# Kernel tuning notes

Measured on AMD Instinct MI355X. Metric: run time of the kernel, lower is better.

## Reference

```python
import jax, jax.numpy as jnp
import numpy as np

EMBED = 1024
HEADS = 16
HEAD_DIM = EMBED // HEADS


def setup_inputs() -> dict:
    key = jax.random.key(0)
    ks = jax.random.split(key, 8)
    B, S = 2, 2048
    inp = {
        "values": jax.random.normal(ks[0], (B, S, EMBED), jnp.float32),
        "keys": jax.random.normal(ks[1], (B, S, EMBED), jnp.float32),
        "queries": jax.random.normal(ks[2], (B, S, EMBED), jnp.float32),
        # per-head projection weights (torch Linear: y = x @ W.T), shared across heads
        "Wv": jax.random.normal(ks[3], (HEAD_DIM, HEAD_DIM), jnp.float32) / np.sqrt(HEAD_DIM),
        "Wk": jax.random.normal(ks[4], (HEAD_DIM, HEAD_DIM), jnp.float32) / np.sqrt(HEAD_DIM),
        "Wq": jax.random.normal(ks[5], (HEAD_DIM, HEAD_DIM), jnp.float32) / np.sqrt(HEAD_DIM),
        "Wo": jax.random.normal(ks[6], (EMBED, EMBED), jnp.float32) / np.sqrt(EMBED),
        "bo": jax.random.normal(ks[7], (EMBED,), jnp.float32) * 0.02,
    }
    return inp


def reference(values, keys, queries, Wv, Wk, Wq, Wo, bo):
    B, S, _ = queries.shape
    # split heads: (B, H, S, D)
    def split(x):
        return x.reshape(B, -1, HEADS, HEAD_DIM).transpose(0, 2, 1, 3)
    v, k, q = split(values), split(keys), split(queries)
    # per-head linear projections (no bias): x @ W.T
    v = jnp.einsum('bhsd,ed->bhse', v, Wv)
    k = jnp.einsum('bhsd,ed->bhse', k, Wk)
    q = jnp.einsum('bhsd,ed->bhse', q, Wq)
    # scaled dot-product attention (naive, full matrix)
    scores = jnp.einsum('bhqd,bhkd->bhqk', q, k) / jnp.sqrt(jnp.float32(HEAD_DIM))
    attn = jax.nn.softmax(scores, axis=-1)
    out = jnp.einsum('bhqk,bhkd->bhqd', attn, v)
    # merge heads and output projection
    out = out.transpose(0, 2, 1, 3).reshape(B, S, EMBED)
    return out @ Wo.T + bo
```

## Files before the change

### kernel.cpp

```cpp
#include <hip/hip_runtime.h>
#include <stdint.h>

#define HEADS 16
#define HD    64
#define SEQ   2048
#define BATCH 2
#define EMB   1024

using short8  = __attribute__((ext_vector_type(8))) short;
using float4v = __attribute__((ext_vector_type(4))) float;
using f32x16  = __attribute__((ext_vector_type(16))) float;

__device__ __forceinline__ unsigned int f2bfr(float f) {
    return (__float_as_uint(f) + 0x8000u) >> 16;
}

__device__ __forceinline__ unsigned int cvt_pk_bf16(float lo, float hi) {
    unsigned int r;
    asm("v_cvt_pk_bf16_f32 %0, %1, %2" : "=v"(r) : "v"(lo), "v"(hi));
    return r;
}

__device__ __forceinline__ short8 mk8(unsigned int a, unsigned int b,
                                      unsigned int c, unsigned int d) {
    union { unsigned int u[4]; short8 s; } x;
    x.u[0] = a; x.u[1] = b; x.u[2] = c; x.u[3] = d;
    return x.s;
}

__global__ __launch_bounds__(256) void cvt_wo_kernel(const float* __restrict__ Wo,
                                                     unsigned short* __restrict__ Wob) {
    int i = (blockIdx.x * 256 + threadIdx.x) * 4;
    float4 v = *(const float4*)(Wo + i);
    uint2 o;
    o.x = f2bfr(v.x) | (f2bfr(v.y) << 16);
    o.y = f2bfr(v.z) | (f2bfr(v.w) << 16);
    *(uint2*)(Wob + i) = o;
}

__global__ __launch_bounds__(256) void proj_kernel(
    const float* __restrict__ Vx, const float* __restrict__ Kx, const float* __restrict__ Qx,
    const float* __restrict__ Wv, const float* __restrict__ Wk, const float* __restrict__ Wq,
    unsigned short* __restrict__ Qp, unsigned short* __restrict__ Kp,
    unsigned short* __restrict__ Vt) {
    __shared__ __align__(16) unsigned short Ws[64 * 72];
    __shared__ __align__(16) unsigned short xs[64 * 72];
    __shared__ __align__(16) unsigned short vt2[64 * 72];

    const int t = threadIdx.x, w = t >> 6, lane = t & 63, cl = lane & 15, quad = lane >> 4;
    const int z  = blockIdx.z;
    const int bh = blockIdx.y;
    const int b  = bh >> 4, h = bh & 15;
    const int s0 = blockIdx.x * 64;

    const float* x = (z == 0) ? Qx : (z == 1) ? Kx : Vx;
    const float* W = (z == 0) ? Wq : (z == 1) ? Wk : Wv;
    const float scale = (z == 0) ? 0.18033688011112044f : 1.0f;

#pragma unroll
    for (int rep = 0; rep < 4; ++rep) {
        int idx = rep * 1024 + t * 4;
        int e = idx >> 6, d0 = idx & 63;
        float4 w4 = *(const float4*)(W + idx);
        uint2 pk;
        pk.x = f2bfr(w4.x * scale) | (f2bfr(w4.y * scale) << 16);
        pk.y = f2bfr(w4.z * scale) | (f2bfr(w4.w * scale) << 16);
        *(uint2*)(&Ws[e * 72 + d0]) = pk;

        int s = e;
        float4 v4 = *(const float4*)(x + (size_t)(b * SEQ + s0 + s) * EMB + h * 64 + d0);
        uint2 px;
        px.x = f2bfr(v4.x) | (f2bfr(v4.y) << 16);
        px.y = f2bfr(v4.z) | (f2bfr(v4.w) << 16);
        *(uint2*)(&xs[s * 72 + d0]) = px;
    }
    __syncthreads();

    short8 a0 = *(const short8*)(&xs[(w * 16 + cl) * 72 + quad * 8]);
    short8 a1 = *(const short8*)(&xs[(w * 16 + cl) * 72 + 32 + quad * 8]);
    float4v c[4];
#pragma unroll
    for (int nt = 0; nt < 4; ++nt) c[nt] = (float4v){0.f, 0.f, 0.f, 0.f};
#pragma unroll
    for (int nt = 0; nt < 4; ++nt) {
        short8 b0 = *(const short8*)(&Ws[(nt * 16 + cl) * 72 + quad * 8]);
        c[nt] = __builtin_amdgcn_mfma_f32_16x16x32_bf16(a0, b0, c[nt], 0, 0, 0);
        short8 b1 = *(const short8*)(&Ws[(nt * 16 + cl) * 72 + 32 + quad * 8]);
        c[nt] = __builtin_amdgcn_mfma_f32_16x16x32_bf16(a1, b1, c[nt], 0, 0, 0);
    }

    if (z < 2) {
#pragma unroll
        for (int nt = 0; nt < 4; ++nt)
#pragma unroll
            for (int r = 0; r < 4; ++r)
                xs[(w * 16 + quad * 4 + r) * 72 + nt * 16 + cl] =
                    (unsigned short)f2bfr(c[nt][r]);
        unsigned short* outp = (z == 0) ? Qp : Kp;
        int sl = w * 16 + (lane >> 2), c0 = (lane & 3) * 16;
        uint4 o0 = *(const uint4*)(&xs[sl * 72 + c0]);
        uint4 o1 = *(const uint4*)(&xs[sl * 72 + c0 + 8]);
        size_t base = ((size_t)bh * SEQ + s0 + sl) * 64 + c0;
        *(uint4*)(outp + base)     = o0;
        *(uint4*)(outp + base + 8) = o1;
    } else {
#pragma unroll
        for (int nt = 0; nt < 4; ++nt)
#pragma unroll
            for (int r = 0; r < 4; ++r)
                vt2[(nt * 16 + cl) * 72 + w * 16 + quad * 4 + r] =
                    (unsigned short)f2bfr(c[nt][r]);
        __syncthreads();
        int e = t >> 2, sc0 = (t & 3) * 16;
        uint4 o0 = *(const uint4*)(&vt2[e * 72 + sc0]);
        uint4 o1 = *(const uint4*)(&vt2[e * 72 + sc0 + 8]);
        size_t base = ((size_t)bh * 64 + e) * SEQ + s0 + sc0;
        *(uint4*)(Vt + base)     = o0;
        *(uint4*)(Vt + base + 8) = o1;
    }
}

__global__ __launch_bounds__(256) void attn_kernel(
    const unsigned short* __restrict__ Qp, const unsigned short* __restrict__ Kp,
    const unsigned short* __restrict__ Vt, unsigned short* __restrict__ AO) {
    __shared__ __align__(16) unsigned short Ks[2][64 * 72];
    __shared__ __align__(16) unsigned short Vs[2][64 * 72];

    const int t = threadIdx.x;
    const int w = t >> 6, lane = t & 63;
    const int l31 = lane & 31, h = lane >> 5;

    const int lid = blockIdx.x;
    const int bh  = ((lid & 7) << 2) | ((lid >> 3) & 3);
    const int q0  = (lid >> 5) * 128;

    const size_t hbase = (size_t)bh * SEQ * 64;
    const unsigned short* Kbase = Kp + hbase;
    const unsigned short* Vbase = Vt + hbase;

    short8 qf[4];
    {
        const unsigned short* qr = Qp + hbase + (size_t)(q0 + w * 32 + l31) * 64 + h * 8;
#pragma unroll
        for (int dt = 0; dt < 4; ++dt) qf[dt] = *(const short8*)(qr + dt * 16);
    }

    short8 ones;
#pragma unroll
    for (int i = 0; i < 8; ++i) ones[i] = (short)0x3F80;

    f32x16 o0, o1, ls;
#pragma unroll
    for (int r = 0; r < 16; ++r) { o0[r] = 0.f; o1[r] = 0.f; ls[r] = 0.f; }

    const int srow = t >> 3;
    const int scol = (t & 7) * 8;

    uint4 kreg[2], vreg[2];
#pragma unroll
    for (int p = 0; p < 2; ++p) {
        int row = srow + p * 32;
        kreg[p] = *(const uint4*)(Kbase + row * 64 + scol);
        vreg[p] = *(const uint4*)(Vbase + (size_t)row * SEQ + scol);
    }

    for (int kc = 0; kc < SEQ / 64; ++kc) {
        const int buf = kc & 1;
#pragma unroll
        for (int p = 0; p < 2; ++p) {
            int row = srow + p * 32;
            *(uint4*)(&Ks[buf][row * 72 + scol]) = kreg[p];
            *(uint4*)(&Vs[buf][row * 72 + scol]) = vreg[p];
        }
        __syncthreads();
        if (kc + 1 < SEQ / 64) {
#pragma unroll
            for (int p = 0; p < 2; ++p) {
                int row = srow + p * 32;
                kreg[p] = *(const uint4*)(Kbase + (size_t)(kc + 1) * 4096 + row * 64 + scol);
                vreg[p] = *(const uint4*)(Vbase + (size_t)row * SEQ + (kc + 1) * 64 + scol);
            }
        }

        f32x16 s0, s1;
#pragma unroll
        for (int r = 0; r < 16; ++r) { s0[r] = 0.f; s1[r] = 0.f; }

        __builtin_amdgcn_s_setprio(1);
#pragma unroll
        for (int dt = 0; dt < 4; ++dt) {
            short8 k0 = *(const short8*)(&Ks[buf][l31 * 72 + dt * 16 + h * 8]);
            short8 k1 = *(const short8*)(&Ks[buf][(32 + l31) * 72 + dt * 16 + h * 8]);
            s0 = __builtin_amdgcn_mfma_f32_32x32x16_bf16(k0, qf[dt], s0, 0, 0, 0);
            s1 = __builtin_amdgcn_mfma_f32_32x32x16_bf16(k1, qf[dt], s1, 0, 0, 0);
        }
        __builtin_amdgcn_s_setprio(0);

#pragma unroll
        for (int r = 0; r < 16; ++r) {
            s0[r] = __builtin_amdgcn_exp2f(s0[r]);
            s1[r] = __builtin_amdgcn_exp2f(s1[r]);
        }

        short8 fr[4];
        {
            unsigned e0 = cvt_pk_bf16(s0[0],  s0[1]),  e1 = cvt_pk_bf16(s0[2],  s0[3]);
            unsigned e2 = cvt_pk_bf16(s0[4],  s0[5]),  e3 = cvt_pk_bf16(s0[6],  s0[7]);
            unsigned e4 = cvt_pk_bf16(s0[8],  s0[9]),  e5 = cvt_pk_bf16(s0[10], s0[11]);
            unsigned e6 = cvt_pk_bf16(s0[12], s0[13]), e7 = cvt_pk_bf16(s0[14], s0[15]);
            unsigned x0 = __shfl_xor(e0, 32), x1 = __shfl_xor(e1, 32);
            unsigned x2 = __shfl_xor(e2, 32), x3 = __shfl_xor(e3, 32);
            unsigned x4 = __shfl_xor(e4, 32), x5 = __shfl_xor(e5, 32);
            unsigned x6 = __shfl_xor(e6, 32), x7 = __shfl_xor(e7, 32);
            fr[0] = mk8(h ? x2 : e0, h ? x3 : e1, h ? e2 : x0, h ? e3 : x1);
            fr[1] = mk8(h ? x6 : e4, h ? x7 : e5, h ? e6 : x4, h ? e7 : x5);
        }
        {
            unsigned e0 = cvt_pk_bf16(s1[0],  s1[1]),  e1 = cvt_pk_bf16(s1[2],  s1[3]);
            unsigned e2 = cvt_pk_bf16(s1[4],  s1[5]),  e3 = cvt_pk_bf16(s1[6],  s1[7]);
            unsigned e4 = cvt_pk_bf16(s1[8],  s1[9]),  e5 = cvt_pk_bf16(s1[10], s1[11]);
            unsigned e6 = cvt_pk_bf16(s1[12], s1[13]), e7 = cvt_pk_bf16(s1[14], s1[15]);
            unsigned x0 = __shfl_xor(e0, 32), x1 = __shfl_xor(e1, 32);
            unsigned x2 = __shfl_xor(e2, 32), x3 = __shfl_xor(e3, 32);
            unsigned x4 = __shfl_xor(e4, 32), x5 = __shfl_xor(e5, 32);
            unsigned x6 = __shfl_xor(e6, 32), x7 = __shfl_xor(e7, 32);
            fr[2] = mk8(h ? x2 : e0, h ? x3 : e1, h ? e2 : x0, h ? e3 : x1);
            fr[3] = mk8(h ? x6 : e4, h ? x7 : e5, h ? e6 : x4, h ? e7 : x5);
        }

        __builtin_amdgcn_s_setprio(1);
#pragma unroll
        for (int c = 0; c < 4; ++c) {
            short8 bv0 = *(const short8*)(&Vs[buf][l31 * 72 + c * 16 + h * 8]);
            short8 bv1 = *(const short8*)(&Vs[buf][(32 + l31) * 72 + c * 16 + h * 8]);
            o0 = __builtin_amdgcn_mfma_f32_32x32x16_bf16(fr[c], bv0, o0, 0, 0, 0);
            o1 = __builtin_amdgcn_mfma_f32_32x32x16_bf16(fr[c], bv1, o1, 0, 0, 0);
            ls = __builtin_amdgcn_mfma_f32_32x32x16_bf16(fr[c], ones,  ls, 0, 0, 0);
        }
        __builtin_amdgcn_s_setprio(0);
    }

    float inv[16];
#pragma unroll
    for (int r = 0; r < 16; ++r) inv[r] = 1.0f / ls[r];
#pragma unroll
    for (int r = 0; r < 16; ++r) {
        int row = q0 + w * 32 + (r & 3) + 8 * (r >> 2) + 4 * h;
        size_t rb = hbase + (size_t)row * 64 + l31;
        AO[rb]      = (unsigned short)f2bfr(o0[r] * inv[r]);
        AO[rb + 32] = (unsigned short)f2bfr(o1[r] * inv[r]);
    }
}

__global__ __launch_bounds__(256) void outproj_kernel(
    const unsigned short* __restrict__ AO, const unsigned short* __restrict__ Wob,
    const float* __restrict__ bo, float* __restrict__ out) {
    const int t = threadIdx.x, w = t >> 6, lane = t & 63;
    const int l31 = lane & 31, h = lane >> 5;

    const int wid = blockIdx.x * 4 + w;
    const int mt  = wid >> 4;
    const int et  = wid & 15;
    const int m0  = mt * 32, e0 = et * 64;
    const int b   = m0 >> 11;
    const int s   = (m0 & 2047) + l31;

    const unsigned short* pA  = AO + ((size_t)(b * 16) * SEQ + s) * 64 + h * 8;
    const unsigned short* pB0 = Wob + (size_t)(e0 + l31) * EMB + h * 8;
    const unsigned short* pB1 = Wob + (size_t)(e0 + 32 + l31) * EMB + h * 8;

    f32x16 c0, c1;
#pragma unroll
    for (int r = 0; r < 16; ++r) { c0[r] = 0.f; c1[r] = 0.f; }

    for (int hh = 0; hh < 16; ++hh) {
#pragma unroll
        for (int k4 = 0; k4 < 4; ++k4) {
            short8 a  = *(const short8*)(pA + k4 * 16);
            short8 b0 = *(const short8*)(pB0 + hh * 64 + k4 * 16);
            short8 b1 = *(const short8*)(pB1 + hh * 64 + k4 * 16);
            c0 = __builtin_amdgcn_mfma_f32_32x32x16_bf16(a, b0, c0, 0, 0, 0);
            c1 = __builtin_amdgcn_mfma_f32_32x32x16_bf16(a, b1, c1, 0, 0, 0);
        }
        pA += (size_t)SEQ * 64;
    }

    const float bias0 = bo[e0 + l31];
    const float bias1 = bo[e0 + 32 + l31];
#pragma unroll
    for (int r = 0; r < 16; ++r) {
        int m = m0 + (r & 3) + 8 * (r >> 2) + 4 * h;
        out[(size_t)m * EMB + e0 + l31]      = c0[r] + bias0;
        out[(size_t)m * EMB + e0 + 32 + l31] = c1[r] + bias1;
    }
}

extern "C" void kernel_launch(void* const* d_in, const int* in_sizes, int n_in,
                              void* d_out, int out_size, void* d_ws, size_t ws_size,
                              hipStream_t stream) {
    const float* values  = (const float*)d_in[0];
    const float* keys    = (const float*)d_in[1];
    const float* queries = (const float*)d_in[2];
    const float* Wv = (const float*)d_in[3];
    const float* Wk = (const float*)d_in[4];
    const float* Wq = (const float*)d_in[5];
    const float* Wo = (const float*)d_in[6];
    const float* bo = (const float*)d_in[7];
    float* out = (float*)d_out;

    char* ws = (char*)d_ws;
    unsigned short* Qp  = (unsigned short*)(ws);
    unsigned short* Kp  = (unsigned short*)(ws + (8u  << 20));
    unsigned short* Vt  = (unsigned short*)(ws + (16u << 20));
    unsigned short* AO  = (unsigned short*)(ws + (24u << 20));
    unsigned short* Wob = (unsigned short*)(ws + (32u << 20));

    cvt_wo_kernel<<<dim3(1024), dim3(256), 0, stream>>>(Wo, Wob);
    proj_kernel<<<dim3(SEQ / 64, BATCH * HEADS, 3), dim3(256), 0, stream>>>(
        values, keys, queries, Wv, Wk, Wq, Qp, Kp, Vt);
    attn_kernel<<<dim3((SEQ / 128) * BATCH * HEADS), dim3(256), 0, stream>>>(Qp, Kp, Vt, AO);
    outproj_kernel<<<dim3((EMB / 64) * ((BATCH * SEQ) / 32) / 4), dim3(256), 0, stream>>>(
        AO, Wob, bo, out);
}
```

Baseline: 231.3 us.

## Rewrite projection kernel as per-wave 32x32 MFMA tiles without shared memory

The projection kernel now gives each wave its own 32-row sequence tile. Each wave loads the input and weight fragments straight from global memory into registers, converts them to bf16 with the packed convert instruction, and uses 32x32x16 MFMAs. This removes the LDS staging, the __syncthreads barriers and the shared-memory transpose for V. In exchange, the outputs are written as scattered 2-byte stores, and every wave reloads the full 64x64 weight matrix from global memory.

```diff
diff --git a/kernel.cpp b/kernel.cpp
--- a/kernel.cpp
+++ b/kernel.cpp
@@ -43,80 +43,78 @@
     const float* __restrict__ Wv, const float* __restrict__ Wk, const float* __restrict__ Wq,
     unsigned short* __restrict__ Qp, unsigned short* __restrict__ Kp,
     unsigned short* __restrict__ Vt) {
-    __shared__ __align__(16) unsigned short Ws[64 * 72];
-    __shared__ __align__(16) unsigned short xs[64 * 72];
-    __shared__ __align__(16) unsigned short vt2[64 * 72];
-
-    const int t = threadIdx.x, w = t >> 6, lane = t & 63, cl = lane & 15, quad = lane >> 4;
-    const int z  = blockIdx.z;
-    const int bh = blockIdx.y;
-    const int b  = bh >> 4, h = bh & 15;
-    const int s0 = blockIdx.x * 64;
+    const int t = threadIdx.x, w = t >> 6, lane = t & 63;
+    const int l31 = lane & 31, h = lane >> 5;
+
+    const int wid  = blockIdx.x * 4 + w;
+    const int z    = wid >> 11;
+    const int rest = wid & 2047;
+    const int bh   = rest >> 6;
+    const int s0   = (rest & 63) * 32;
+    const int b    = bh >> 4, hh = bh & 15;
 
     const float* x = (z == 0) ? Qx : (z == 1) ? Kx : Vx;
     const float* W = (z == 0) ? Wq : (z == 1) ? Wk : Wv;
     const float scale = (z == 0) ? 0.18033688011112044f : 1.0f;
 
-#pragma unroll
-    for (int rep = 0; rep < 4; ++rep) {
-        int idx = rep * 1024 + t * 4;
-        int e = idx >> 6, d0 = idx & 63;
-        float4 w4 = *(const float4*)(W + idx);
-        uint2 pk;
-        pk.x = f2bfr(w4.x * scale) | (f2bfr(w4.y * scale) << 16);
-        pk.y = f2bfr(w4.z * scale) | (f2bfr(w4.w * scale) << 16);
-        *(uint2*)(&Ws[e * 72 + d0]) = pk;
-
-        int s = e;
-        float4 v4 = *(const float4*)(x + (size_t)(b * SEQ + s0 + s) * EMB + h * 64 + d0);
-        uint2 px;
-        px.x = f2bfr(v4.x) | (f2bfr(v4.y) << 16);
-        px.y = f2bfr(v4.z) | (f2bfr(v4.w) << 16);
-        *(uint2*)(&xs[s * 72 + d0]) = px;
-    }
-    __syncthreads();
-
-    short8 a0 = *(const short8*)(&xs[(w * 16 + cl) * 72 + quad * 8]);
-    short8 a1 = *(const short8*)(&xs[(w * 16 + cl) * 72 + 32 + quad * 8]);
-    float4v c[4];
-#pragma unroll
-    for (int nt = 0; nt < 4; ++nt) c[nt] = (float4v){0.f, 0.f, 0.f, 0.f};
-#pragma unroll
-    for (int nt = 0; nt < 4; ++nt) {
-        short8 b0 = *(const short8*)(&Ws[(nt * 16 + cl) * 72 + quad * 8]);
-        c[nt] = __builtin_amdgcn_mfma_f32_16x16x32_bf16(a0, b0, c[nt], 0, 0, 0);
-        short8 b1 = *(const short8*)(&Ws[(nt * 16 + cl) * 72 + 32 + quad * 8]);
-        c[nt] = __builtin_amdgcn_mfma_f32_16x16x32_bf16(a1, b1, c[nt], 0, 0, 0);
-    }
+    const float* xr = x + ((size_t)(b * SEQ + s0 + l31)) * EMB + hh * 64 + h * 8;
+    short8 xf[4];
+#pragma unroll
+    for (int dt = 0; dt < 4; ++dt) {
+        const float* p = xr + dt * 16;
+        float4 u = *(const float4*)p;
+        float4 v = *(const float4*)(p + 4);
+        xf[dt] = mk8(cvt_pk_bf16(u.x, u.y), cvt_pk_bf16(u.z, u.w),
+                     cvt_pk_bf16(v.x, v.y), cvt_pk_bf16(v.z, v.w));
+    }
+
+    short8 wf[2][4];
+#pragma unroll
+    for (int et = 0; et < 2; ++et) {
+        const float* wr = W + (size_t)(et * 32 + l31) * 64 + h * 8;
+#pragma unroll
+        for (int dt = 0; dt < 4; ++dt) {
+            const float* p = wr + dt * 16;
+            float4 u = *(const float4*)p;
+            float4 v = *(const float4*)(p + 4);
+            wf[et][dt] = mk8(cvt_pk_bf16(u.x * scale, u.y * scale),
+                             cvt_pk_bf16(u.z * scale, u.w * scale),
+                             cvt_pk_bf16(v.x * scale, v.y * scale),
+                             cvt_pk_bf16(v.z * scale, v.w * scale));
+        }
+    }
+
+    f32x16 c0, c1;
+#pragma unroll
+    for (int r = 0; r < 16; ++r) { c0[r] = 0.f; c1[r] = 0.f; }
 
     if (z < 2) {
 #pragma unroll
-        for (int nt = 0; nt < 4; ++nt)
-#pragma unroll
-            for (int r = 0; r < 4; ++r)
-                xs[(w * 16 + quad * 4 + r) * 72 + nt * 16 + cl] =
-                    (unsigned short)f2bfr(c[nt][r]);
+        for (int dt = 0; dt < 4; ++dt) {
+            c0 = __builtin_amdgcn_mfma_f32_32x32x16_bf16(xf[dt], wf[0][dt], c0, 0, 0, 0);
+            c1 = __builtin_amdgcn_mfma_f32_32x32x16_bf16(xf[dt], wf[1][dt], c1, 0, 0, 0);
+        }
         unsigned short* outp = (z == 0) ? Qp : Kp;
-        int sl = w * 16 + (lane >> 2), c0 = (lane & 3) * 16;
-        uint4 o0 = *(const uint4*)(&xs[sl * 72 + c0]);
-        uint4 o1 = *(const uint4*)(&xs[sl * 72 + c0 + 8]);
-        size_t base = ((size_t)bh * SEQ + s0 + sl) * 64 + c0;
-        *(uint4*)(outp + base)     = o0;
-        *(uint4*)(outp + base + 8) = o1;
+        size_t base = ((size_t)bh * SEQ + s0) * 64;
+#pragma unroll
+        for (int r = 0; r < 16; ++r) {
+            int sr = (r & 3) + 8 * (r >> 2) + 4 * h;
+            outp[base + (size_t)sr * 64 + l31]      = (unsigned short)f2bfr(c0[r]);
+            outp[base + (size_t)sr * 64 + 32 + l31] = (unsigned short)f2bfr(c1[r]);
+        }
     } else {
 #pragma unroll
-        for (int nt = 0; nt < 4; ++nt)
-#pragma unroll
-            for (int r = 0; r < 4; ++r)
-                vt2[(nt * 16 + cl) * 72 + w * 16 + quad * 4 + r] =
-                    (unsigned short)f2bfr(c[nt][r]);
-        __syncthreads();
-        int e = t >> 2, sc0 = (t & 3) * 16;
-        uint4 o0 = *(const uint4*)(&vt2[e * 72 + sc0]);
-        uint4 o1 = *(const uint4*)(&vt2[e * 72 + sc0 + 8]);
-        size_t base = ((size_t)bh * 64 + e) * SEQ + s0 + sc0;
-        *(uint4*)(Vt + base)     = o0;
-        *(uint4*)(Vt + base + 8) = o1;
+        for (int dt = 0; dt < 4; ++dt) {
+            c0 = __builtin_amdgcn_mfma_f32_32x32x16_bf16(wf[0][dt], xf[dt], c0, 0, 0, 0);
+            c1 = __builtin_amdgcn_mfma_f32_32x32x16_bf16(wf[1][dt], xf[dt], c1, 0, 0, 0);
+        }
+        size_t base = (size_t)bh * 64 * SEQ + s0;
+#pragma unroll
+        for (int r = 0; r < 16; ++r) {
+            int er = (r & 3) + 8 * (r >> 2) + 4 * h;
+            Vt[base + (size_t)er * SEQ + l31]        = (unsigned short)f2bfr(c0[r]);
+            Vt[base + (size_t)(32 + er) * SEQ + l31] = (unsigned short)f2bfr(c1[r]);
+        }
     }
 }
 
@@ -316,7 +314,7 @@
     unsigned short* Wob = (unsigned short*)(ws + (32u << 20));
 
     cvt_wo_kernel<<<dim3(1024), dim3(256), 0, stream>>>(Wo, Wob);
-    proj_kernel<<<dim3(SEQ / 64, BATCH * HEADS, 3), dim3(256), 0, stream>>>(
+    proj_kernel<<<dim3(3 * BATCH * HEADS * (SEQ / 32) / 4), dim3(256), 0, stream>>>(
         values, keys, queries, Wv, Wk, Wq, Qp, Kp, Vt);
     attn_kernel<<<dim3((SEQ / 128) * BATCH * HEADS), dim3(256), 0, stream>>>(Qp, Kp, Vt, AO);
     outproj_kernel<<<dim3((EMB / 64) * ((BATCH * SEQ) / 32) / 4), dim3(256), 0, stream>>>(
```

Result: slower. 240.4 us (+3.9%).
